# Kernel tuning notes

Hardware: AMD Instinct MI355X
Metric: run time of the kernel (lower is better)

The kernel has to match this reference:

```python
import jax, jax.numpy as jnp
import numpy as np

B, S, D, F, E = 2, 2048, 1024, 4096, 8
LN_EPS = 1e-5


def setup_inputs() -> dict:
    key = jax.random.key(0)
    ks = jax.random.split(key, 8)
    def xavier(k, shape):
        fan_in, fan_out = shape[-1], shape[-2]
        a = jnp.sqrt(6.0 / (fan_in + fan_out))
        return jax.random.uniform(k, shape, jnp.float32, -a, a)
    return {
        "tgt": jax.random.normal(ks[0], (B, S, D), jnp.float32),
        "Wr": xavier(ks[1], (E, D)),          # router weight
        "br": jnp.zeros((E,), jnp.float32),    # router bias
        "W1": xavier(ks[2], (E, F, D)),        # expert up-proj
        "b1": jnp.zeros((E, F), jnp.float32),
        "W2": xavier(ks[3], (E, D, F)),        # expert down-proj
        "b2": jnp.zeros((E, D), jnp.float32),
        "gamma": jnp.ones((D,), jnp.float32),  # LayerNorm weight
        "beta": jnp.zeros((D,), jnp.float32),  # LayerNorm bias
    }


def _layer_norm(x, gamma, beta):
    mu = jnp.mean(x, axis=-1, keepdims=True)
    var = jnp.mean(jnp.square(x - mu), axis=-1, keepdims=True)
    return (x - mu) * jax.lax.rsqrt(var + LN_EPS) * gamma + beta


def reference(tgt, Wr, br, W1, b1, W2, b2, gamma, beta):
    # Top-2 sparse router weights (renormalized softmax over the top-2 logits)
    logits = jnp.einsum('bsd,ed->bse', tgt, Wr) + br            # [B,S,E]
    top_v, top_i = jax.lax.top_k(logits, 2)                      # [B,S,2]
    top_w = jax.nn.softmax(top_v, axis=-1)                       # [B,S,2]
    n_exp = logits.shape[-1]
    # scatter top-2 weights back to dense [B,S,E] (zeros elsewhere)
    router_w = jnp.sum(jax.nn.one_hot(top_i, n_exp, dtype=top_w.dtype)
                       * top_w[..., None], axis=-2)              # [B,S,E]

    # Dense all-experts FFN (faithful to the original loop over experts)
    h = jnp.einsum('bsd,efd->bsef', tgt, W1) + b1                # [B,S,E,F]
    h = jax.nn.relu(h)
    o = jnp.einsum('bsef,edf->bsed', h, W2) + b2                 # [B,S,E,D]
    tgt2 = jnp.einsum('bsed,bse->bsd', o, router_w)              # weighted combine

    # residual + post-norm (dropout=0.0 -> identity)
    return _layer_norm(tgt + tgt2, gamma, beta)
```

## Files before the change

### kernel.cpp

```cpp
#include <hip/hip_runtime.h>
#include <hip/hip_bf16.h>

#define B_ 2
#define S_ 2048
#define D_ 1024
#define F_ 4096
#define E_ 8
#define NTOK (B_*S_)
#define NPAIR (2*NTOK)
#define LN_EPS 1e-5f

#define BM 128
#define BN 128
#define BK 64
#define PAD 8
#define LDW (BK + PAD)

typedef short bf16x8 __attribute__((ext_vector_type(8)));
typedef float f32x4 __attribute__((ext_vector_type(4)));

static constexpr size_t WS_COUNTS  = 0;
static constexpr size_t WS_CURSORS = 256;
static constexpr size_t WS_OFFSETS = 512;
static constexpr size_t WS_FLAG    = 960;
static constexpr size_t WS_TOKE    = 1280;
static constexpr size_t WS_TOKW    = WS_TOKE + 4ull*NTOK;
static constexpr size_t WS_PTOK    = WS_TOKW + 8ull*NTOK;
static constexpr size_t WS_PDEST   = WS_PTOK + 4ull*NPAIR;
static constexpr size_t WS_PW      = WS_PDEST + 4ull*NPAIR;
static constexpr size_t WS_HBUF    = ((WS_PW + 4ull*NPAIR + 255)/256)*256;
static constexpr size_t WS_W1C     = WS_HBUF + 2ull*NPAIR*F_;
static constexpr size_t WS_OBUF    = WS_W1C;
static constexpr size_t WS_W2C     = WS_W1C + 2ull*E_*F_*D_;
static constexpr size_t WS_XC      = WS_W2C + 2ull*E_*D_*F_;
static constexpr size_t WS_BIG_END = WS_XC  + 2ull*NTOK*D_;
static constexpr size_t WS_SMALL_END = WS_OBUF + 4ull*NPAIR*D_;

__device__ __forceinline__ float ldin(const void* p, size_t i, bool f32) {
    return f32 ? ((const float*)p)[i]
               : __bfloat162float(((const __hip_bfloat16*)p)[i]);
}

__device__ __forceinline__ void stage8(short* dst, const void* src, size_t off, bool f32) {
    if (f32) {
        const float* s = (const float*)src + off;
        const float4 a = *(const float4*)s;
        const float4 b = *(const float4*)(s + 4);
        union { short sh[8]; uint4 v; } u;
        __hip_bfloat16* h = (__hip_bfloat16*)u.sh;
        h[0] = __float2bfloat16(a.x); h[1] = __float2bfloat16(a.y);
        h[2] = __float2bfloat16(a.z); h[3] = __float2bfloat16(a.w);
        h[4] = __float2bfloat16(b.x); h[5] = __float2bfloat16(b.y);
        h[6] = __float2bfloat16(b.z); h[7] = __float2bfloat16(b.w);
        *(uint4*)dst = u.v;
    } else {
        *(uint4*)dst = *(const uint4*)((const __hip_bfloat16*)src + off);
    }
}

__device__ __forceinline__ uint4 pack8(const float4& a, const float4& b) {
    union { short sh[8]; uint4 v; } u;
    __hip_bfloat16* h = (__hip_bfloat16*)u.sh;
    h[0] = __float2bfloat16(a.x); h[1] = __float2bfloat16(a.y);
    h[2] = __float2bfloat16(a.z); h[3] = __float2bfloat16(a.w);
    h[4] = __float2bfloat16(b.x); h[5] = __float2bfloat16(b.y);
    h[6] = __float2bfloat16(b.z); h[7] = __float2bfloat16(b.w);
    return u.v;
}

__device__ __forceinline__ void glds16(const void* g, void* l) {
    __builtin_amdgcn_global_load_lds(
        (const __attribute__((address_space(1))) unsigned int*)g,
        (__attribute__((address_space(3))) unsigned int*)l, 16, 0, 0);
}

__global__ void moe_detect(const unsigned* __restrict__ gamma_raw, int* __restrict__ flag,
                           int* __restrict__ counts, int* __restrict__ cursors)
{
    const int t = threadIdx.x;
    if (t == 0) *flag = (gamma_raw[0] == 0x3F800000u) ? 1 : 0;
    if (t < E_) { counts[t] = 0; cursors[t] = 0; }
}

__global__ __launch_bounds__(256) void moe_convert_w(
    const void* __restrict__ w1, const void* __restrict__ w2,
    __hip_bfloat16* __restrict__ d1, __hip_bfloat16* __restrict__ d2,
    const int* __restrict__ flagp)
{
    const bool f32 = flagp[0] != 0;
    const long n8    = (long)E_ * F_ * D_ / 8;
    const long total = 2 * n8;
    const long stride = (long)gridDim.x * 256;
    long i = (long)blockIdx.x * 256 + threadIdx.x;

    for (; i + 3*stride < total; i += 4*stride) {
        long idx[4];
        #pragma unroll
        for (int u = 0; u < 4; ++u) idx[u] = i + u*stride;
        if (f32) {
            float4 a[4], b[4];
            #pragma unroll
            for (int u = 0; u < 4; ++u) {
                const float* s = (idx[u] < n8)
                    ? (const float*)w1 + idx[u]*8
                    : (const float*)w2 + (idx[u]-n8)*8;
                a[u] = *(const float4*)s;
                b[u] = *(const float4*)(s + 4);
            }
            #pragma unroll
            for (int u = 0; u < 4; ++u) {
                const uint4 v = pack8(a[u], b[u]);
                __hip_bfloat16* dst = (idx[u] < n8) ? d1 + idx[u]*8
                                                    : d2 + (idx[u]-n8)*8;
                *(uint4*)dst = v;
            }
        } else {
            uint4 v[4];
            #pragma unroll
            for (int u = 0; u < 4; ++u) {
                const __hip_bfloat16* s = (idx[u] < n8)
                    ? (const __hip_bfloat16*)w1 + idx[u]*8
                    : (const __hip_bfloat16*)w2 + (idx[u]-n8)*8;
                v[u] = *(const uint4*)s;
            }
            #pragma unroll
            for (int u = 0; u < 4; ++u) {
                __hip_bfloat16* dst = (idx[u] < n8) ? d1 + idx[u]*8
                                                    : d2 + (idx[u]-n8)*8;
                *(uint4*)dst = v[u];
            }
        }
    }
    for (; i < total; i += stride) {
        if (i < n8) stage8((short*)(d1 + i*8), w1, (size_t)i*8, f32);
        else        stage8((short*)(d2 + (i-n8)*8), w2, (size_t)(i-n8)*8, f32);
    }
}

__global__ __launch_bounds__(256) void moe_router(
    const void* __restrict__ X, const void* __restrict__ Wr, const void* __restrict__ br,
    const int* __restrict__ flagp,
    int* __restrict__ toke, float2* __restrict__ tokw,
    __hip_bfloat16* __restrict__ Xc)
{
    const bool f32 = flagp[0] != 0;
    const int wv   = threadIdx.x >> 6;
    const int lane = threadIdx.x & 63;
    const int t    = blockIdx.x * 4 + wv;

    float acc[E_];
    #pragma unroll
    for (int e = 0; e < E_; ++e) acc[e] = 0.f;

    if (f32) {
        const float* Xf  = (const float*)X;
        const float* Wrf = (const float*)Wr;
        for (int i = 0; i < D_/64; ++i) {
            const int d = i*64 + lane;
            const float x = Xf[(size_t)t*D_ + d];
            if (Xc) Xc[(size_t)t*D_ + d] = __float2bfloat16(x);
            #pragma unroll
            for (int e = 0; e < E_; ++e) acc[e] += x * Wrf[e*D_ + d];
        }
    } else {
        const __hip_bfloat16* Xb  = (const __hip_bfloat16*)X;
        const __hip_bfloat16* Wrb = (const __hip_bfloat16*)Wr;
        for (int i = 0; i < D_/64; ++i) {
            const int d = i*64 + lane;
            const __hip_bfloat16 xb = Xb[(size_t)t*D_ + d];
            if (Xc) Xc[(size_t)t*D_ + d] = xb;
            const float x = __bfloat162float(xb);
            #pragma unroll
            for (int e = 0; e < E_; ++e) acc[e] += x * __bfloat162float(Wrb[e*D_ + d]);
        }
    }
    #pragma unroll
    for (int e = 0; e < E_; ++e) {
        #pragma unroll
        for (int s = 32; s; s >>= 1) acc[e] += __shfl_xor(acc[e], s);
        acc[e] += ldin(br, e, f32);
    }
    int e0 = 0; float v0 = acc[0];
    #pragma unroll
    for (int e = 1; e < E_; ++e) if (acc[e] > v0) { v0 = acc[e]; e0 = e; }
    int e1 = (e0 == 0) ? 1 : 0; float v1 = -1e30f;
    #pragma unroll
    for (int e = 0; e < E_; ++e) if (e != e0 && acc[e] > v1) { v1 = acc[e]; e1 = e; }
    const float ex = __expf(v1 - v0);
    const float w0 = 1.f / (1.f + ex);
    const float w1 = ex / (1.f + ex);

    if (lane == 0) {
        toke[t] = e0 | (e1 << 8);
        tokw[t] = make_float2(w0, w1);
    }
}

__global__ __launch_bounds__(256) void moe_count(const int* __restrict__ toke,
                                                 int* __restrict__ counts)
{
    const int tid = threadIdx.x;
    int c[E_];
    #pragma unroll
    for (int e = 0; e < E_; ++e) c[e] = 0;
    for (int t = tid; t < NTOK; t += 256) {
        const int ee = toke[t];
        const int e0 = ee & 0xff, e1 = (ee >> 8) & 0xff;
        #pragma unroll
        for (int e = 0; e < E_; ++e) c[e] += (e0 == e) + (e1 == e);
    }
    #pragma unroll
    for (int e = 0; e < E_; ++e) {
        #pragma unroll
        for (int s = 32; s; s >>= 1) c[e] += __shfl_xor(c[e], s);
    }
    __shared__ int red[4][E_];
    const int wv = tid >> 6, lane = tid & 63;
    if (lane == 0) {
        #pragma unroll
        for (int e = 0; e < E_; ++e) red[wv][e] = c[e];
    }
    __syncthreads();
    if (tid < E_)
        counts[tid] = red[0][tid] + red[1][tid] + red[2][tid] + red[3][tid];
}

__global__ __launch_bounds__(256) void moe_build_lists(
    const int* __restrict__ toke, const float2* __restrict__ tokw,
    const int* __restrict__ counts, int* __restrict__ offsets, int* __restrict__ cursors,
    int* __restrict__ ptok, int* __restrict__ pdest, float* __restrict__ pw)
{
    __shared__ int lcnt[E_], lbase[E_], loffs[E_ + 1];
    const int tid = threadIdx.x;
    if (tid < E_) lcnt[tid] = 0;
    if (tid == 0) {
        int s = 0;
        #pragma unroll
        for (int e = 0; e < E_; ++e) { loffs[e] = s; s += counts[e]; }
        loffs[E_] = s;
        if (blockIdx.x == 0) {
            #pragma unroll
            for (int e = 0; e <= E_; ++e) offsets[e] = loffs[e];
        }
    }
    __syncthreads();

    const int t = blockIdx.x * 256 + tid;
    const int ee = toke[t];
    const float2 w = tokw[t];
    const int e0 = ee & 0xff, e1 = (ee >> 8) & 0xff;
    const int r0 = atomicAdd(&lcnt[e0], 1);
    const int r1 = atomicAdd(&lcnt[e1], 1);
    __syncthreads();
    if (tid < E_) lbase[tid] = atomicAdd(&cursors[tid], lcnt[tid]);
    __syncthreads();

    const int p0 = loffs[e0] + lbase[e0] + r0;
    ptok[p0] = t; pdest[p0] = 2*t;     pw[p0] = w.x;
    const int p1 = loffs[e1] + lbase[e1] + r1;
    ptok[p1] = t; pdest[p1] = 2*t + 1; pw[p1] = w.y;
}


__global__ __launch_bounds__(256, 3) void moe_up_gemm_g(
    const __hip_bfloat16* __restrict__ X,
    const __hip_bfloat16* __restrict__ W1,
    const void* __restrict__ b1p,
    const int* __restrict__ biasflag,
    const int* __restrict__ offsets,
    const int* __restrict__ ptok,
    __hip_bfloat16* __restrict__ H)
{
    const bool bf32 = biasflag[0] != 0;
    const int e  = blockIdx.z;
    const int off = offsets[e];
    const int ne  = offsets[e+1] - off;
    const int m0  = blockIdx.y * BM;
    if (m0 >= ne) return;
    const int n0  = blockIdx.x * BN;

    __shared__ __align__(16) short As[BM*BK];
    __shared__ __align__(16) short Bs[BN*BK];
    __shared__ int toks[BM];

    const int tid = threadIdx.x;
    if (tid < BM) {
        int m = m0 + tid;
        toks[tid] = ptok[off + (m < ne ? m : ne - 1)];
    }
    __syncthreads();

    const int w = tid >> 6, lane = tid & 63;
    const int wm = (w & 1) * 64, wn = (w >> 1) * 64;
    const int lrow = lane & 15, lq = lane >> 4;

    const __hip_bfloat16* gA[4]; const __hip_bfloat16* gB[4];
    short *lA[4], *lB[4];
    #pragma unroll
    for (int t = 0; t < 4; ++t) {
        const int chunk = (w*4 + t)*64 + lane;
        const int row = chunk >> 3, c8 = chunk & 7;
        const int csw = (c8 ^ (row & 7)) * 8;
        gA[t] = X  + (size_t)toks[row]*D_ + csw;
        gB[t] = W1 + ((size_t)e*F_ + n0 + row)*D_ + csw;
        lA[t] = &As[chunk*8];
        lB[t] = &Bs[chunk*8];
    }
    int offA[4], offB[4];
    #pragma unroll
    for (int i = 0; i < 4; ++i) {
        offA[i] = (wm + i*16 + lrow) * BK;
        offB[i] = (wn + i*16 + lrow) * BK;
    }

    f32x4 acc[4][4] = {};

    for (int k0 = 0; k0 < D_; k0 += BK) {
        #pragma unroll
        for (int t = 0; t < 4; ++t) {
            glds16(gA[t] + k0, lA[t]);
            glds16(gB[t] + k0, lB[t]);
        }
        __syncthreads();
        #pragma unroll
        for (int ks = 0; ks < 2; ++ks) {
            const int csw = ((ks*4 + lq) ^ (lrow & 7)) * 8;
            bf16x8 a[4], b[4];
            #pragma unroll
            for (int i = 0; i < 4; ++i) {
                a[i] = *(const bf16x8*)&As[offA[i] + csw];
                b[i] = *(const bf16x8*)&Bs[offB[i] + csw];
            }
            #pragma unroll
            for (int i = 0; i < 4; ++i)
                #pragma unroll
                for (int j = 0; j < 4; ++j)
                    acc[i][j] = __builtin_amdgcn_mfma_f32_16x16x32_bf16(a[i], b[j], acc[i][j], 0,0,0);
        }
        __syncthreads();
    }

    float bias[4];
    #pragma unroll
    for (int j = 0; j < 4; ++j)
        bias[j] = ldin(b1p, (size_t)e*F_ + n0 + wn + j*16 + lrow, bf32);

    #pragma unroll
    for (int i = 0; i < 4; ++i) {
        #pragma unroll
        for (int r = 0; r < 4; ++r) {
            const int m = m0 + wm + i*16 + lq*4 + r;
            if (m < ne) {
                #pragma unroll
                for (int j = 0; j < 4; ++j) {
                    const int f = n0 + wn + j*16 + lrow;
                    float v = acc[i][j][r] + bias[j];
                    v = v > 0.f ? v : 0.f;
                    H[(size_t)(off + m)*F_ + f] = __float2bfloat16(v);
                }
            }
        }
    }
}

__global__ __launch_bounds__(256, 3) void moe_down_gemm_g(
    const __hip_bfloat16* __restrict__ H,
    const __hip_bfloat16* __restrict__ W2,
    const void* __restrict__ b2p,
    const int* __restrict__ biasflag,
    const int* __restrict__ offsets,
    const int* __restrict__ pdest,
    const float* __restrict__ pw,
    float* __restrict__ O)
{
    const bool bf32 = biasflag[0] != 0;
    const int nb  = gridDim.x;
    const int swz = (blockIdx.x & 7) * (nb >> 3) + (blockIdx.x >> 3);
    const int GX = D_/BN, GY = NTOK/BM;
    const int e   = swz / (GX*GY);
    const int rem = swz % (GX*GY);
    const int m0  = (rem / GX) * BM;
    const int n0  = (rem % GX) * BN;

    const int off = offsets[e];
    const int ne  = offsets[e+1] - off;
    if (m0 >= ne) return;

    __shared__ __align__(16) short As[BM*BK];
    __shared__ __align__(16) short Bs[BN*BK];

    const int tid = threadIdx.x;
    const int w = tid >> 6, lane = tid & 63;
    const int wm = (w & 1) * 64, wn = (w >> 1) * 64;
    const int lrow = lane & 15, lq = lane >> 4;

    const __hip_bfloat16* gA[4]; const __hip_bfloat16* gB[4];
    short *lA[4], *lB[4];
    #pragma unroll
    for (int t = 0; t < 4; ++t) {
        const int chunk = (w*4 + t)*64 + lane;
        const int row = chunk >> 3, c8 = chunk & 7;
        const int csw = (c8 ^ (row & 7)) * 8;
        const int mm = m0 + row;
        const int p  = off + (mm < ne ? mm : ne - 1);
        gA[t] = H + (size_t)p*F_ + csw;
        gB[t] = W2 + ((size_t)e*D_ + n0 + row)*F_ + csw;
        lA[t] = &As[chunk*8];
        lB[t] = &Bs[chunk*8];
    }
    int offA[4], offB[4];
    #pragma unroll
    for (int i = 0; i < 4; ++i) {
        offA[i] = (wm + i*16 + lrow) * BK;
        offB[i] = (wn + i*16 + lrow) * BK;
    }

    f32x4 acc[4][4] = {};

    for (int k0 = 0; k0 < F_; k0 += BK) {
        #pragma unroll
        for (int t = 0; t < 4; ++t) {
            glds16(gA[t] + k0, lA[t]);
            glds16(gB[t] + k0, lB[t]);
        }
        __syncthreads();
        #pragma unroll
        for (int ks = 0; ks < 2; ++ks) {
            const int csw = ((ks*4 + lq) ^ (lrow & 7)) * 8;
            bf16x8 a[4], b[4];
            #pragma unroll
            for (int i = 0; i < 4; ++i) {
                a[i] = *(const bf16x8*)&As[offA[i] + csw];
                b[i] = *(const bf16x8*)&Bs[offB[i] + csw];
            }
            #pragma unroll
            for (int i = 0; i < 4; ++i)
                #pragma unroll
                for (int j = 0; j < 4; ++j)
                    acc[i][j] = __builtin_amdgcn_mfma_f32_16x16x32_bf16(a[i], b[j], acc[i][j], 0,0,0);
        }
        __syncthreads();
    }

    float bias[4];
    #pragma unroll
    for (int j = 0; j < 4; ++j)
        bias[j] = ldin(b2p, (size_t)e*D_ + n0 + wn + j*16 + lrow, bf32);

    #pragma unroll
    for (int i = 0; i < 4; ++i) {
        #pragma unroll
        for (int r = 0; r < 4; ++r) {
            const int m = m0 + wm + i*16 + lq*4 + r;
            if (m < ne) {
                const int p = off + m;
                const size_t orow = (size_t)pdest[p]*D_;
                const float wgt = pw[p];
                #pragma unroll
                for (int j = 0; j < 4; ++j) {
                    const int d = n0 + wn + j*16 + lrow;
                    O[orow + d] = (acc[i][j][r] + bias[j]) * wgt;
                }
            }
        }
    }
}

__global__ __launch_bounds__(256, 2) void moe_up_gemm(
    const void* __restrict__ X, const void* __restrict__ W1, const void* __restrict__ b1p,
    const int* __restrict__ srcflag, const int* __restrict__ biasflag,
    const int* __restrict__ offsets, const int* __restrict__ ptok,
    __hip_bfloat16* __restrict__ H)
{
    const bool sf32 = srcflag[0] != 0;
    const bool bf32 = biasflag[0] != 0;
    const int e  = blockIdx.z;
    const int off = offsets[e];
    const int ne  = offsets[e+1] - off;
    const int m0  = blockIdx.y * BM;
    if (m0 >= ne) return;
    const int n0  = blockIdx.x * BN;

    __shared__ __align__(16) short As[BM][LDW];
    __shared__ __align__(16) short Bs[BN][LDW];
    __shared__ int toks[BM];

    const int tid = threadIdx.x;
    if (tid < BM) {
        int m = m0 + tid;
        toks[tid] = ptok[off + (m < ne ? m : ne - 1)];
    }
    __syncthreads();

    const int w = tid >> 6, lane = tid & 63;
    const int wm = (w & 1) * 64, wn = (w >> 1) * 64;
    const int lrow = lane & 15, lq = lane >> 4;

    f32x4 acc[4][4] = {};

    for (int k0 = 0; k0 < D_; k0 += BK) {
        #pragma unroll
        for (int j = 0; j < 4; ++j) {
            const int idx = tid + j*256;
            const int r = idx >> 3, c = (idx & 7) * 8;
            stage8(&As[r][c], X,  (size_t)toks[r]*D_ + k0 + c, sf32);
            stage8(&Bs[r][c], W1, ((size_t)e*F_ + n0 + r)*D_ + k0 + c, sf32);
        }
        __syncthreads();
        #pragma unroll
        for (int ks = 0; ks < 2; ++ks) {
            bf16x8 a[4], b[4];
            #pragma unroll
            for (int i = 0; i < 4; ++i) {
                a[i] = *(const bf16x8*)&As[wm + i*16 + lrow][ks*32 + lq*8];
                b[i] = *(const bf16x8*)&Bs[wn + i*16 + lrow][ks*32 + lq*8];
            }
            #pragma unroll
            for (int i = 0; i < 4; ++i)
                #pragma unroll
                for (int j = 0; j < 4; ++j)
                    acc[i][j] = __builtin_amdgcn_mfma_f32_16x16x32_bf16(a[i], b[j], acc[i][j], 0,0,0);
        }
        __syncthreads();
    }

    #pragma unroll
    for (int i = 0; i < 4; ++i) {
        #pragma unroll
        for (int r = 0; r < 4; ++r) {
            const int m = m0 + wm + i*16 + lq*4 + r;
            if (m < ne) {
                #pragma unroll
                for (int j = 0; j < 4; ++j) {
                    const int f = n0 + wn + j*16 + lrow;
                    float v = acc[i][j][r] + ldin(b1p, e*F_ + f, bf32);
                    v = v > 0.f ? v : 0.f;
                    H[(size_t)(off + m)*F_ + f] = __float2bfloat16(v);
                }
            }
        }
    }
}

__global__ __launch_bounds__(256, 2) void moe_down_gemm(
    const __hip_bfloat16* __restrict__ H,
    const void* __restrict__ W2, const void* __restrict__ b2p,
    const int* __restrict__ srcflag, const int* __restrict__ biasflag,
    const int* __restrict__ offsets, const int* __restrict__ pdest,
    const float* __restrict__ pw, float* __restrict__ O)
{
    const bool sf32 = srcflag[0] != 0;
    const bool bf32 = biasflag[0] != 0;
    const int e  = blockIdx.z;
    const int off = offsets[e];
    const int ne  = offsets[e+1] - off;
    const int m0  = blockIdx.y * BM;
    if (m0 >= ne) return;
    const int n0  = blockIdx.x * BN;

    __shared__ __align__(16) short As[BM][LDW];
    __shared__ __align__(16) short Bs[BN][LDW];

    const int tid = threadIdx.x;
    const int w = tid >> 6, lane = tid & 63;
    const int wm = (w & 1) * 64, wn = (w >> 1) * 64;
    const int lrow = lane & 15, lq = lane >> 4;

    f32x4 acc[4][4] = {};

    for (int k0 = 0; k0 < F_; k0 += BK) {
        #pragma unroll
        for (int j = 0; j < 4; ++j) {
            const int idx = tid + j*256;
            const int r = idx >> 3, c = (idx & 7) * 8;
            const int mm = m0 + r;
            const int p  = off + (mm < ne ? mm : ne - 1);
            *(uint4*)&As[r][c] = *(const uint4*)(H + (size_t)p*F_ + k0 + c);
            stage8(&Bs[r][c], W2, ((size_t)e*D_ + n0 + r)*F_ + k0 + c, sf32);
        }
        __syncthreads();
        #pragma unroll
        for (int ks = 0; ks < 2; ++ks) {
            bf16x8 a[4], b[4];
            #pragma unroll
            for (int i = 0; i < 4; ++i) {
                a[i] = *(const bf16x8*)&As[wm + i*16 + lrow][ks*32 + lq*8];
                b[i] = *(const bf16x8*)&Bs[wn + i*16 + lrow][ks*32 + lq*8];
            }
            #pragma unroll
            for (int i = 0; i < 4; ++i)
                #pragma unroll
                for (int j = 0; j < 4; ++j)
                    acc[i][j] = __builtin_amdgcn_mfma_f32_16x16x32_bf16(a[i], b[j], acc[i][j], 0,0,0);
        }
        __syncthreads();
    }

    #pragma unroll
    for (int i = 0; i < 4; ++i) {
        #pragma unroll
        for (int r = 0; r < 4; ++r) {
            const int m = m0 + wm + i*16 + lq*4 + r;
            if (m < ne) {
                const int p = off + m;
                const size_t orow = (size_t)pdest[p]*D_;
                const float wgt = pw[p];
                #pragma unroll
                for (int j = 0; j < 4; ++j) {
                    const int d = n0 + wn + j*16 + lrow;
                    O[orow + d] = (acc[i][j][r] + ldin(b2p, e*D_ + d, bf32)) * wgt;
                }
            }
        }
    }
}

__global__ __launch_bounds__(256) void moe_combine_ln(
    const void* __restrict__ X, const float* __restrict__ O,
    const void* __restrict__ gamma, const void* __restrict__ beta,
    const int* __restrict__ flagp, void* __restrict__ out)
{
    const bool f32 = flagp[0] != 0;
    const int t = blockIdx.x;
    const int tid = threadIdx.x;
    const int d0 = tid * 4;
    const float* o0 = O + (size_t)(2*t) * D_;
    const float* o1 = o0 + D_;
    float4 a = *(const float4*)(o0 + d0);
    float4 b = *(const float4*)(o1 + d0);

    float x[4];
    float sum = 0.f, ssq = 0.f;
    #pragma unroll
    for (int i = 0; i < 4; ++i) {
        const float xv = ((const float*)&a)[i] + ((const float*)&b)[i]
                       + ldin(X, (size_t)t*D_ + d0 + i, f32);
        x[i] = xv; sum += xv; ssq += xv*xv;
    }
    #pragma unroll
    for (int s = 32; s; s >>= 1) { sum += __shfl_xor(sum, s); ssq += __shfl_xor(ssq, s); }

    __shared__ float red[2][4];
    const int wv = tid >> 6, lane = tid & 63;
    if (lane == 0) { red[0][wv] = sum; red[1][wv] = ssq; }
    __syncthreads();
    sum = red[0][0] + red[0][1] + red[0][2] + red[0][3];
    ssq = red[1][0] + red[1][1] + red[1][2] + red[1][3];
    const float mu   = sum * (1.f/D_);
    const float var  = ssq * (1.f/D_) - mu*mu;
    const float rstd = rsqrtf(var + LN_EPS);

    #pragma unroll
    for (int i = 0; i < 4; ++i) {
        const int d = d0 + i;
        const float y = (x[i] - mu) * rstd * ldin(gamma, d, f32) + ldin(beta, d, f32);
        if (f32) ((float*)out)[(size_t)t*D_ + d] = y;
        else     ((__hip_bfloat16*)out)[(size_t)t*D_ + d] = __float2bfloat16(y);
    }
}

extern "C" void kernel_launch(void* const* d_in, const int* in_sizes, int n_in,
                              void* d_out, int out_size, void* d_ws, size_t ws_size,
                              hipStream_t stream)
{
    const void* tgt   = d_in[0];
    const void* Wr    = d_in[1];
    const void* br    = d_in[2];
    const void* W1    = d_in[3];
    const void* b1    = d_in[4];
    const void* W2    = d_in[5];
    const void* b2    = d_in[6];
    const void* gamma = d_in[7];
    const void* beta  = d_in[8];

    char* ws = (char*)d_ws;
    int*      counts  = (int*)(ws + WS_COUNTS);
    int*      cursors = (int*)(ws + WS_CURSORS);
    int*      offsets = (int*)(ws + WS_OFFSETS);
    int*      flag    = (int*)(ws + WS_FLAG);
    int*      toke    = (int*)(ws + WS_TOKE);
    float2*   tokw    = (float2*)(ws + WS_TOKW);
    int*      ptok    = (int*)(ws + WS_PTOK);
    int*      pdest   = (int*)(ws + WS_PDEST);
    float*    pw      = (float*)(ws + WS_PW);
    __hip_bfloat16* hbuf = (__hip_bfloat16*)(ws + WS_HBUF);
    float*    obuf    = (float*)(ws + WS_OBUF);
    __hip_bfloat16* W1c  = (__hip_bfloat16*)(ws + WS_W1C);
    __hip_bfloat16* W2c  = (__hip_bfloat16*)(ws + WS_W2C);
    __hip_bfloat16* Xc   = (__hip_bfloat16*)(ws + WS_XC);

    moe_detect<<<1, 64, 0, stream>>>((const unsigned*)gamma, flag, counts, cursors);

    const bool big = ws_size >= WS_BIG_END;
    if (big)
        moe_convert_w<<<8192, 256, 0, stream>>>(W1, W2, W1c, W2c, flag);

    moe_router<<<NTOK/4, 256, 0, stream>>>(tgt, Wr, br, flag, toke, tokw,
                                           big ? Xc : (__hip_bfloat16*)nullptr);
    moe_count<<<1, 256, 0, stream>>>(toke, counts);
    moe_build_lists<<<NTOK/256, 256, 0, stream>>>(toke, tokw, counts, offsets, cursors,
                                                  ptok, pdest, pw);

    if (big) {
        moe_up_gemm_g<<<dim3(F_/BN, NTOK/BM, E_), 256, 0, stream>>>(
            Xc, W1c, b1, flag, offsets, ptok, hbuf);
        moe_down_gemm_g<<<(D_/BN)*(NTOK/BM)*E_, 256, 0, stream>>>(
            hbuf, W2c, b2, flag, offsets, pdest, pw, obuf);
    } else {
        moe_up_gemm<<<dim3(F_/BN, NTOK/BM, E_), 256, 0, stream>>>(
            tgt, W1, b1, flag, flag, offsets, ptok, hbuf);
        moe_down_gemm<<<dim3(D_/BN, NTOK/BM, E_), 256, 0, stream>>>(
            hbuf, W2, b2, flag, flag, offsets, pdest, pw, obuf);
    }
    moe_combine_ln<<<NTOK, 256, 0, stream>>>(tgt, obuf, gamma, beta, flag, d_out);
}
```

Measured before the change: 547.6 us.

## Overlap weight bf16 conversion with router and up-GEMM kernels via extra blocks

Removes the standalone weight-conversion kernel and splits its work: W1 conversion runs as extra blocks appended to the router launch, and W2 conversion runs as extra blocks appended to the up-projection GEMM launch (which now uses a flattened 1D grid). The intent is to hide the bandwidth-bound conversion behind the router and the many early-exiting GEMM tiles instead of serialising it. The trade-off is that conversion blocks compete with GEMM blocks for CUs and bandwidth, and correctness relies on stream ordering placing W2 conversion before the down GEMM.

```diff
diff --git a/kernel.cpp b/kernel.cpp
--- a/kernel.cpp
+++ b/kernel.cpp
@@ -68,6 +68,40 @@
     return u.v;
 }
 
+__device__ __forceinline__ void convert_tensor(
+    const void* __restrict__ src, __hip_bfloat16* __restrict__ dst,
+    long n8, long tid0, long stride, bool f32)
+{
+    long i = tid0;
+    for (; i + 3*stride < n8; i += 4*stride) {
+        long idx[4];
+        #pragma unroll
+        for (int u = 0; u < 4; ++u) idx[u] = i + u*stride;
+        if (f32) {
+            float4 a[4], b[4];
+            #pragma unroll
+            for (int u = 0; u < 4; ++u) {
+                const float* s = (const float*)src + idx[u]*8;
+                a[u] = *(const float4*)s;
+                b[u] = *(const float4*)(s + 4);
+            }
+            #pragma unroll
+            for (int u = 0; u < 4; ++u)
+                *(uint4*)(dst + idx[u]*8) = pack8(a[u], b[u]);
+        } else {
+            uint4 v[4];
+            #pragma unroll
+            for (int u = 0; u < 4; ++u)
+                v[u] = *(const uint4*)((const __hip_bfloat16*)src + idx[u]*8);
+            #pragma unroll
+            for (int u = 0; u < 4; ++u)
+                *(uint4*)(dst + idx[u]*8) = v[u];
+        }
+    }
+    for (; i < n8; i += stride)
+        stage8((short*)(dst + i*8), src, (size_t)i*8, f32);
+}
+
 __device__ __forceinline__ void glds16(const void* g, void* l) {
     __builtin_amdgcn_global_load_lds(
         (const __attribute__((address_space(1))) unsigned int*)g,
@@ -82,68 +116,24 @@
     if (t < E_) { counts[t] = 0; cursors[t] = 0; }
 }
 
-__global__ __launch_bounds__(256) void moe_convert_w(
-    const void* __restrict__ w1, const void* __restrict__ w2,
-    __hip_bfloat16* __restrict__ d1, __hip_bfloat16* __restrict__ d2,
-    const int* __restrict__ flagp)
-{
-    const bool f32 = flagp[0] != 0;
-    const long n8    = (long)E_ * F_ * D_ / 8;
-    const long total = 2 * n8;
-    const long stride = (long)gridDim.x * 256;
-    long i = (long)blockIdx.x * 256 + threadIdx.x;
-
-    for (; i + 3*stride < total; i += 4*stride) {
-        long idx[4];
-        #pragma unroll
-        for (int u = 0; u < 4; ++u) idx[u] = i + u*stride;
-        if (f32) {
-            float4 a[4], b[4];
-            #pragma unroll
-            for (int u = 0; u < 4; ++u) {
-                const float* s = (idx[u] < n8)
-                    ? (const float*)w1 + idx[u]*8
-                    : (const float*)w2 + (idx[u]-n8)*8;
-                a[u] = *(const float4*)s;
-                b[u] = *(const float4*)(s + 4);
-            }
-            #pragma unroll
-            for (int u = 0; u < 4; ++u) {
-                const uint4 v = pack8(a[u], b[u]);
-                __hip_bfloat16* dst = (idx[u] < n8) ? d1 + idx[u]*8
-                                                    : d2 + (idx[u]-n8)*8;
-                *(uint4*)dst = v;
-            }
-        } else {
-            uint4 v[4];
-            #pragma unroll
-            for (int u = 0; u < 4; ++u) {
-                const __hip_bfloat16* s = (idx[u] < n8)
-                    ? (const __hip_bfloat16*)w1 + idx[u]*8
-                    : (const __hip_bfloat16*)w2 + (idx[u]-n8)*8;
-                v[u] = *(const uint4*)s;
-            }
-            #pragma unroll
-            for (int u = 0; u < 4; ++u) {
-                __hip_bfloat16* dst = (idx[u] < n8) ? d1 + idx[u]*8
-                                                    : d2 + (idx[u]-n8)*8;
-                *(uint4*)dst = v[u];
-            }
-        }
-    }
-    for (; i < total; i += stride) {
-        if (i < n8) stage8((short*)(d1 + i*8), w1, (size_t)i*8, f32);
-        else        stage8((short*)(d2 + (i-n8)*8), w2, (size_t)(i-n8)*8, f32);
-    }
-}
-
-__global__ __launch_bounds__(256) void moe_router(
+__global__ __launch_bounds__(256) void moe_router_cvt1(
     const void* __restrict__ X, const void* __restrict__ Wr, const void* __restrict__ br,
     const int* __restrict__ flagp,
     int* __restrict__ toke, float2* __restrict__ tokw,
-    __hip_bfloat16* __restrict__ Xc)
+    __hip_bfloat16* __restrict__ Xc,
+    const void* __restrict__ w1, __hip_bfloat16* __restrict__ d1)
 {
     const bool f32 = flagp[0] != 0;
+    const int nrb = NTOK/4;
+
+    if ((int)blockIdx.x >= nrb) {
+        const long n8 = (long)E_ * F_ * D_ / 8;
+        const long stride = (long)(gridDim.x - nrb) * 256;
+        const long tid0 = (long)(blockIdx.x - nrb)*256 + threadIdx.x;
+        convert_tensor(w1, d1, n8, tid0, stride, f32);
+        return;
+    }
+
     const int wv   = threadIdx.x >> 6;
     const int lane = threadIdx.x & 63;
     const int t    = blockIdx.x * 4 + wv;
@@ -188,11 +178,11 @@
     for (int e = 0; e < E_; ++e) if (e != e0 && acc[e] > v1) { v1 = acc[e]; e1 = e; }
     const float ex = __expf(v1 - v0);
     const float w0 = 1.f / (1.f + ex);
-    const float w1 = ex / (1.f + ex);
+    const float w1v = ex / (1.f + ex);
 
     if (lane == 0) {
         toke[t] = e0 | (e1 << 8);
-        tokw[t] = make_float2(w0, w1);
+        tokw[t] = make_float2(w0, w1v);
     }
 }
 
@@ -262,22 +252,36 @@
 }
 
 
-__global__ __launch_bounds__(256, 3) void moe_up_gemm_g(
+__global__ __launch_bounds__(256, 3) void moe_up_cvt2(
     const __hip_bfloat16* __restrict__ X,
     const __hip_bfloat16* __restrict__ W1,
     const void* __restrict__ b1p,
     const int* __restrict__ biasflag,
     const int* __restrict__ offsets,
     const int* __restrict__ ptok,
-    __hip_bfloat16* __restrict__ H)
+    __hip_bfloat16* __restrict__ H,
+    const void* __restrict__ w2, __hip_bfloat16* __restrict__ d2)
 {
     const bool bf32 = biasflag[0] != 0;
-    const int e  = blockIdx.z;
+    const int GX = F_/BN, GY = NTOK/BM;
+    const int nub = GX*GY*E_;
+
+    if ((int)blockIdx.x >= nub) {
+        const long n8 = (long)E_ * D_ * F_ / 8;
+        const long stride = (long)(gridDim.x - nub) * 256;
+        const long tid0 = (long)(blockIdx.x - nub)*256 + threadIdx.x;
+        convert_tensor(w2, d2, n8, tid0, stride, bf32);
+        return;
+    }
+
+    const int e   = blockIdx.x / (GX*GY);
+    const int rem = blockIdx.x % (GX*GY);
+    const int m0  = (rem / GX) * BM;
+    const int n0  = (rem % GX) * BN;
+
     const int off = offsets[e];
     const int ne  = offsets[e+1] - off;
-    const int m0  = blockIdx.y * BM;
     if (m0 >= ne) return;
-    const int n0  = blockIdx.x * BN;
 
     __shared__ __align__(16) short As[BM*BK];
     __shared__ __align__(16) short Bs[BN*BK];
@@ -692,18 +696,22 @@
     moe_detect<<<1, 64, 0, stream>>>((const unsigned*)gamma, flag, counts, cursors);
 
     const bool big = ws_size >= WS_BIG_END;
-    if (big)
-        moe_convert_w<<<8192, 256, 0, stream>>>(W1, W2, W1c, W2c, flag);
-
-    moe_router<<<NTOK/4, 256, 0, stream>>>(tgt, Wr, br, flag, toke, tokw,
-                                           big ? Xc : (__hip_bfloat16*)nullptr);
+
+    if (big) {
+        moe_router_cvt1<<<NTOK/4 + 4096, 256, 0, stream>>>(
+            tgt, Wr, br, flag, toke, tokw, Xc, W1, W1c);
+    } else {
+        moe_router_cvt1<<<NTOK/4, 256, 0, stream>>>(
+            tgt, Wr, br, flag, toke, tokw, (__hip_bfloat16*)nullptr,
+            nullptr, (__hip_bfloat16*)nullptr);
+    }
     moe_count<<<1, 256, 0, stream>>>(toke, counts);
     moe_build_lists<<<NTOK/256, 256, 0, stream>>>(toke, tokw, counts, offsets, cursors,
                                                   ptok, pdest, pw);
 
     if (big) {
-        moe_up_gemm_g<<<dim3(F_/BN, NTOK/BM, E_), 256, 0, stream>>>(
-            Xc, W1c, b1, flag, offsets, ptok, hbuf);
+        moe_up_cvt2<<<(F_/BN)*(NTOK/BM)*E_ + 4096, 256, 0, stream>>>(
+            Xc, W1c, b1, flag, offsets, ptok, hbuf, W2, W2c);
         moe_down_gemm_g<<<(D_/BN)*(NTOK/BM)*E_, 256, 0, stream>>>(
             hbuf, W2c, b2, flag, offsets, pdest, pw, obuf);
     } else {
```

After: 529.9 us. 3.2% less time.
